# Optimization experiments

Hardware: AMD Instinct MI355X
Metric: run time of the kernel (lower is better)

Reference implementation:

```python
import jax, jax.numpy as jnp
import numpy as np

N = 100000
IN_DIM = 128
HID = 32
HEADS = 2
DEG = 16
NEG_SLOPE = 0.2


def setup_inputs() -> dict:
    rng = np.random.default_rng(0)
    E_rand = N * DEG
    src = np.concatenate([rng.integers(0, N, E_rand), np.arange(N)]).astype(np.int64)
    dst = np.concatenate([rng.integers(0, N, E_rand), np.arange(N)]).astype(np.int64)

    key = jax.random.key(0)
    ks = jax.random.split(key, 10)
    feat = jax.random.normal(ks[0], (N, IN_DIM), dtype=jnp.float32)
    # layer 1: in_dim -> HEADS * HID
    W1 = jax.random.normal(ks[1], (IN_DIM, HEADS * HID), dtype=jnp.float32) / np.sqrt(IN_DIM)
    al1 = jax.random.normal(ks[2], (HEADS, HID), dtype=jnp.float32) * 0.1
    ar1 = jax.random.normal(ks[3], (HEADS, HID), dtype=jnp.float32) * 0.1
    b1 = jnp.zeros((HEADS * HID,), dtype=jnp.float32)
    # layer 2: HEADS*HID -> 1 * HID
    W2 = jax.random.normal(ks[4], (HEADS * HID, HID), dtype=jnp.float32) / np.sqrt(HEADS * HID)
    al2 = jax.random.normal(ks[5], (1, HID), dtype=jnp.float32) * 0.1
    ar2 = jax.random.normal(ks[6], (1, HID), dtype=jnp.float32) * 0.1
    b2 = jnp.zeros((HID,), dtype=jnp.float32)
    return {"feat": feat, "W1": W1, "al1": al1, "ar1": ar1, "b1": b1,
            "W2": W2, "al2": al2, "ar2": ar2, "b2": b2,
            "src": jnp.asarray(src), "dst": jnp.asarray(dst)}


def gat_conv(feat, W, al, ar, b, src, dst, n_nodes, activation=True):
    # DGL GATConv: fc (no bias) -> per-head dot with attn vecs -> leaky_relu
    # edge score -> softmax over incoming edges of each dst -> scatter-add -> +bias -> relu
    H, D = al.shape
    h = (feat @ W).reshape(-1, H, D)                       # [N,H,D]
    el = jnp.einsum('nhd,hd->nh', h, al)                   # [N,H]
    er = jnp.einsum('nhd,hd->nh', h, ar)                   # [N,H]
    e = jax.nn.leaky_relu(el[src] + er[dst], NEG_SLOPE)    # [E,H]
    m = jax.ops.segment_max(e, dst, num_segments=n_nodes)  # [N,H]
    e = jnp.exp(e - jax.lax.stop_gradient(m)[dst])
    s = jax.ops.segment_sum(e, dst, num_segments=n_nodes)  # [N,H]
    a = e / s[dst]                                         # [E,H]
    msg = h[src] * a[:, :, None]                           # [E,H,D]
    out = jax.ops.segment_sum(msg, dst, num_segments=n_nodes)  # [N,H,D]
    out = out + b.reshape(1, H, D)
    return jax.nn.relu(out) if activation else out


def reference(feat, W1, al1, ar1, b1, W2, al2, ar2, b2, src, dst):
    h = gat_conv(feat, W1, al1, ar1, b1, src, dst, N)      # [N,HEADS,HID]
    h = h.reshape(h.shape[0], -1)                          # [N,HEADS*HID]
    h = gat_conv(h, W2, al2, ar2, b2, src, dst, N)         # [N,1,HID]
    return h.squeeze(1)                                    # [N,HID]
```

## Files before the change

### kernel.cpp

```cpp
#include <hip/hip_runtime.h>
#include <hip/hip_fp16.h>
#include <math.h>


constexpr int CAP  = 64;
constexpr int MAXB = 512;
constexpr int TILE = 2048;
constexpr int BCAP = 5120;

typedef _Float16 f16x8 __attribute__((ext_vector_type(8)));
typedef float    f32x4 __attribute__((ext_vector_type(4)));

__global__ __launch_bounds__(256)
void k_prew(const float* __restrict__ W1, const float* __restrict__ al1, const float* __restrict__ ar1,
            const float* __restrict__ W2, const float* __restrict__ al2, const float* __restrict__ ar2,
            _Float16* __restrict__ vh1, _Float16* __restrict__ B2h, int* __restrict__ gcur)
{
    const int t = threadIdx.x;
    for (int i = t; i < 128 * 16; i += 256) {
        const int k = i >> 4, c = i & 15;
        float s = 0.f;
        if (c < 4) {
            const int h = c & 1;
            const float* a = (c >> 1) ? ar1 : al1;
            #pragma unroll
            for (int d = 0; d < 32; d++) s += W1[k * 64 + h * 32 + d] * a[h * 32 + d];
        }
        vh1[i] = (_Float16)s;
    }
    for (int i = t; i < 64 * 64; i += 256) {
        const int k = i >> 6, c = i & 63;
        float s = 0.f;
        if (c < 32) s = W2[k * 32 + c];
        else if (c < 34) {
            const float* a = (c == 32) ? al2 : ar2;
            #pragma unroll
            for (int d = 0; d < 32; d++) s += W2[k * 32 + d] * a[d];
        }
        B2h[i] = (_Float16)s;
    }
    for (int b = t; b < MAXB; b += 256) gcur[b] = 0;
}

__global__ __launch_bounds__(256)
void k_front(const int* __restrict__ src, const int* __restrict__ dst,
             int* __restrict__ gcur, unsigned* __restrict__ binbuf, int E, int Gbin,
             const float* __restrict__ x, const float* __restrict__ W,
             const _Float16* __restrict__ vh1,
             __half* __restrict__ h1, float* __restrict__ el, float* __restrict__ er,
             int nnodes)
{
    __shared__ alignas(16) char smem[32 * 1024];
    const int tid = threadIdx.x;

    if ((int)blockIdx.x < Gbin) {
        int* cnt  = (int*)smem;
        int* base = cnt + MAXB;
        for (int b = tid; b < MAXB; b += 256) cnt[b] = 0;
        __syncthreads();
        const int e0 = blockIdx.x * TILE;
        int lo[8]; unsigned rec[8]; int bn[8];
        #pragma unroll
        for (int u = 0; u < 8; u++) {
            const int e = e0 + u * 256 + tid;
            if (e < E) {
                const int d = dst[e];
                bn[u]  = d >> 8;
                rec[u] = ((unsigned)src[e] << 8) | (unsigned)(d & 255);
                lo[u]  = atomicAdd(&cnt[bn[u]], 1);
            } else bn[u] = -1;
        }
        __syncthreads();
        for (int b = tid; b < MAXB; b += 256) {
            const int c = cnt[b];
            base[b] = c ? atomicAdd(&gcur[b], c) : 0;
        }
        __syncthreads();
        #pragma unroll
        for (int u = 0; u < 8; u++) if (bn[u] >= 0) {
            const int p = base[bn[u]] + lo[u];
            if ((unsigned)p < (unsigned)BCAP)
                binbuf[(long)bn[u] * BCAP + p] = rec[u];
        }
        return;
    }

    _Float16* xs = (_Float16*)smem;
    _Float16* Wh = xs + 64 * 128;
    const int node0 = ((int)blockIdx.x - Gbin) * 64;

    for (int c = tid; c < 1024; c += 256) {
        const int row = c >> 4, k8 = c & 15;
        const int n = node0 + row;
        float4 v0 = make_float4(0, 0, 0, 0), v1 = v0;
        if (n < nnodes) {
            v0 = ((const float4*)x)[(long)n * 32 + k8 * 2];
            v1 = ((const float4*)x)[(long)n * 32 + k8 * 2 + 1];
        }
        f16x8 h;
        h[0] = v0.x; h[1] = v0.y; h[2] = v0.z; h[3] = v0.w;
        h[4] = v1.x; h[5] = v1.y; h[6] = v1.z; h[7] = v1.w;
        const int off = (row * 256 + k8 * 16) ^ ((row & 7) << 4);
        *(f16x8*)((char*)xs + off) = h;
    }
    for (int c = tid; c < 1024; c += 256) {
        const int k = c >> 3, j8 = (c & 7) * 8;
        float4 v0 = ((const float4*)W)[(k * 64 + j8) >> 2];
        float4 v1 = ((const float4*)W)[((k * 64 + j8) >> 2) + 1];
        f16x8 h;
        h[0] = v0.x; h[1] = v0.y; h[2] = v0.z; h[3] = v0.w;
        h[4] = v1.x; h[5] = v1.y; h[6] = v1.z; h[7] = v1.w;
        *(f16x8*)(Wh + k * 64 + j8) = h;
    }
    __syncthreads();

    const int wv = tid >> 6, l = tid & 63;
    const int col = wv * 16 + (l & 15);
    const int g = l >> 4;
    f16x8 bfr[4], vfr[4];
    #pragma unroll
    for (int t = 0; t < 4; t++)
        #pragma unroll
        for (int e = 0; e < 8; e++)
            bfr[t][e] = Wh[(t * 32 + g * 8 + e) * 64 + col];
    if (wv == 0) {
        #pragma unroll
        for (int t = 0; t < 4; t++)
            #pragma unroll
            for (int e = 0; e < 8; e++)
                vfr[t][e] = vh1[(t * 32 + g * 8 + e) * 16 + (l & 15)];
    }

    #pragma unroll
    for (int nt = 0; nt < 4; nt++) {
        f32x4 acc = {0.f, 0.f, 0.f, 0.f}, accv = {0.f, 0.f, 0.f, 0.f};
        const int row = nt * 16 + (l & 15);
        #pragma unroll
        for (int t = 0; t < 4; t++) {
            const int off = (row * 256 + (t * 32 + g * 8) * 2) ^ ((row & 7) << 4);
            f16x8 af = *(const f16x8*)((const char*)xs + off);
            acc = __builtin_amdgcn_mfma_f32_16x16x32_f16(af, bfr[t], acc, 0, 0, 0);
            if (wv == 0)
                accv = __builtin_amdgcn_mfma_f32_16x16x32_f16(af, vfr[t], accv, 0, 0, 0);
        }
        #pragma unroll
        for (int r = 0; r < 4; r++) {
            const int n = node0 + nt * 16 + g * 4 + r;
            if (n < nnodes) {
                h1[(long)n * 64 + col] = __float2half((float)acc[r]);
                if (wv == 0) {
                    const int c4 = l & 15;
                    if (c4 < 2)      el[n * 2 + c4]       = (float)accv[r];
                    else if (c4 < 4) er[n * 2 + (c4 - 2)] = (float)accv[r];
                }
            }
        }
    }
}

__global__ __launch_bounds__(256)
void k_scatter(const unsigned* __restrict__ binbuf, const int* __restrict__ gcur,
               int* __restrict__ deg, int* __restrict__ bucket, int nnodes)
{
    extern __shared__ int lds[];
    int* ldeg  = lds;
    int* lbuck = lds + 256;
    const int t = threadIdx.x, b = blockIdx.x;
    const int nb0 = b << 8;
    ldeg[t] = 0;
    __syncthreads();
    const int cnt = min(max(gcur[b], 0), BCAP);
    const unsigned* recs = binbuf + (long)b * BCAP;
    for (int i = t; i < cnt; i += 256) {
        const unsigned r = recs[i];
        const int nl  = (int)(r & 255u);
        const int pos = atomicAdd(&ldeg[nl], 1);
        if (pos < CAP) lbuck[nl * CAP + pos] = (int)(r >> 8);
    }
    __syncthreads();
    const int nv = min(256, nnodes - nb0);
    if (t < nv) deg[nb0 + t] = ldeg[t];
    const int tot4 = nv * (CAP / 4);
    int4* gb = (int4*)(bucket + (long)nb0 * CAP);
    const int4* lb = (const int4*)lbuck;
    for (int i = t; i < tot4; i += 256) gb[i] = lb[i];
}

__global__ __launch_bounds__(256)
void k_agg1(const __half* __restrict__ hbuf, const float* __restrict__ el,
            const float* __restrict__ er, const int* __restrict__ deg,
            const int* __restrict__ bucket, const float* __restrict__ b1,
            __half* __restrict__ o1, int nnodes)
{
    constexpr int OUT = 64;
    const int w = threadIdx.x >> 6, lane = threadIdx.x & 63;
    const int n = blockIdx.x * 4 + w;
    __shared__ int    sbuf[4][CAP];
    __shared__ float2 wbuf[4][CAP];
    if (n >= nnodes) return;

    const int dn = min(deg[n], CAP);
    const int sv = (lane < dn) ? bucket[(long)n * CAP + lane] : 0;
    sbuf[w][lane] = sv;

    const float2 ernv = ((const float2*)er)[n];
    const float2 elv  = ((const float2*)el)[sv];
    float e0 = elv.x + ernv.x; e0 = (e0 > 0.f) ? e0 : 0.2f * e0;
    float e1 = elv.y + ernv.y; e1 = (e1 > 0.f) ? e1 : 0.2f * e1;
    const float w0 = (lane < dn) ? __expf(e0) : 0.f;
    const float w1 = (lane < dn) ? __expf(e1) : 0.f;
    wbuf[w][lane] = make_float2(w0, w1);
    float s0 = w0, s1 = w1;
    #pragma unroll
    for (int off = 32; off; off >>= 1) {
        s0 += __shfl_xor(s0, off, 64);
        s1 += __shfl_xor(s1, off, 64);
    }
    const float inv0 = (s0 > 0.f) ? 1.f / s0 : 0.f;
    const float inv1 = (s1 > 0.f) ? 1.f / s1 : 0.f;

    const int q = lane >> 3, c8 = lane & 7, hh = c8 >> 2;
    const float invC = hh ? inv1 : inv0;
    float acc[8] = {0.f,0.f,0.f,0.f,0.f,0.f,0.f,0.f};
    for (int i = 0; i < dn; i += 16) {
        const int   sA = sbuf[w][i + q],                     sB = sbuf[w][i + 8 + q];
        const float wA = ((const float*)&wbuf[w][i + q])[hh];
        const float wB = ((const float*)&wbuf[w][i + 8 + q])[hh];
        union { float4 f4; __half2 h2v[4]; } uA, uB;
        uA.f4 = *(const float4*)(hbuf + (long)sA * OUT + c8 * 8);
        uB.f4 = *(const float4*)(hbuf + (long)sB * OUT + c8 * 8);
        #pragma unroll
        for (int j = 0; j < 4; j++) {
            const float2 xa = __half22float2(uA.h2v[j]);
            const float2 xb = __half22float2(uB.h2v[j]);
            acc[2*j]   = fmaf(xa.x, wA, acc[2*j]);
            acc[2*j+1] = fmaf(xa.y, wA, acc[2*j+1]);
            acc[2*j]   = fmaf(xb.x, wB, acc[2*j]);
            acc[2*j+1] = fmaf(xb.y, wB, acc[2*j+1]);
        }
    }
    #pragma unroll
    for (int j = 0; j < 8; j++) {
        acc[j] += __shfl_xor(acc[j], 8, 64);
        acc[j] += __shfl_xor(acc[j], 16, 64);
        acc[j] += __shfl_xor(acc[j], 32, 64);
    }
    if (q == 0) {
        f16x8 ov;
        #pragma unroll
        for (int j = 0; j < 8; j++)
            ov[j] = (_Float16)fmaxf(acc[j] * invC + b1[c8 * 8 + j], 0.f);
        *(f16x8*)((char*)o1 + (long)n * 128 + c8 * 16) = ov;
    }
}

__global__ __launch_bounds__(256)
void k_gemm2(const __half* __restrict__ o1, const _Float16* __restrict__ B2h,
             __half* __restrict__ h2, float* __restrict__ el2, float* __restrict__ er2,
             int nnodes)
{
    __shared__ _Float16 xs[64 * 64];
    const int tid = threadIdx.x;
    const int node0 = blockIdx.x * 64;

    for (int c = tid; c < 512; c += 256) {
        const int row = c >> 3, k8 = c & 7;
        const int n = node0 + row;
        f16x8 h = {0,0,0,0,0,0,0,0};
        if (n < nnodes) h = *(const f16x8*)((const char*)o1 + (long)n * 128 + k8 * 16);
        const int off = (row * 128 + k8 * 16) ^ ((row & 7) << 4);
        *(f16x8*)((char*)xs + off) = h;
    }
    __syncthreads();

    const int wv = tid >> 6, l = tid & 63;
    if (wv == 3) return;
    const int col = wv * 16 + (l & 15);
    const int g = l >> 4;
    f16x8 bfr[2];
    #pragma unroll
    for (int t = 0; t < 2; t++)
        #pragma unroll
        for (int e = 0; e < 8; e++)
            bfr[t][e] = B2h[(t * 32 + g * 8 + e) * 64 + col];

    #pragma unroll
    for (int nt = 0; nt < 4; nt++) {
        f32x4 acc = {0.f, 0.f, 0.f, 0.f};
        const int row = nt * 16 + (l & 15);
        #pragma unroll
        for (int t = 0; t < 2; t++) {
            const int off = (row * 128 + (t * 32 + g * 8) * 2) ^ ((row & 7) << 4);
            f16x8 af = *(const f16x8*)((const char*)xs + off);
            acc = __builtin_amdgcn_mfma_f32_16x16x32_f16(af, bfr[t], acc, 0, 0, 0);
        }
        #pragma unroll
        for (int r = 0; r < 4; r++) {
            const int n = node0 + nt * 16 + g * 4 + r;
            if (n < nnodes) {
                if (wv < 2) h2[(long)n * 32 + col] = __float2half((float)acc[r]);
                else {
                    const int c4 = l & 15;
                    if (c4 == 0)      el2[n] = (float)acc[r];
                    else if (c4 == 1) er2[n] = (float)acc[r];
                }
            }
        }
    }
}

__global__ __launch_bounds__(256)
void k_agg2(const __half* __restrict__ h2, const float* __restrict__ el2,
            const float* __restrict__ er2, const int* __restrict__ deg,
            const int* __restrict__ bucket, const float* __restrict__ b2,
            float* __restrict__ out, int nnodes)
{
    const int w = threadIdx.x >> 6, lane = threadIdx.x & 63;
    const int n = blockIdx.x * 4 + w;
    __shared__ int   sbuf[4][CAP];
    __shared__ float wbuf[4][CAP];
    if (n >= nnodes) return;

    const int dn = min(deg[n], CAP);
    const int sv = (lane < dn) ? bucket[(long)n * CAP + lane] : 0;
    sbuf[w][lane] = sv;

    const float ern = er2[n];
    float e = el2[sv] + ern; e = (e > 0.f) ? e : 0.2f * e;
    const float wt = (lane < dn) ? __expf(e) : 0.f;
    wbuf[w][lane] = wt;
    float s = wt;
    #pragma unroll
    for (int off = 32; off; off >>= 1) s += __shfl_xor(s, off, 64);
    const float inv = (s > 0.f) ? 1.f / s : 0.f;

    const int q = lane >> 2, c8 = lane & 3;
    float acc[8] = {0.f,0.f,0.f,0.f,0.f,0.f,0.f,0.f};
    for (int i = 0; i < dn; i += 16) {
        const int   sA = sbuf[w][i + q];
        const float wA = wbuf[w][i + q];
        union { float4 f4; __half2 h2v[4]; } uA;
        uA.f4 = *(const float4*)(h2 + (long)sA * 32 + c8 * 8);
        #pragma unroll
        for (int j = 0; j < 4; j++) {
            const float2 xa = __half22float2(uA.h2v[j]);
            acc[2*j]   = fmaf(xa.x, wA, acc[2*j]);
            acc[2*j+1] = fmaf(xa.y, wA, acc[2*j+1]);
        }
    }
    #pragma unroll
    for (int j = 0; j < 8; j++) {
        acc[j] += __shfl_xor(acc[j], 4, 64);
        acc[j] += __shfl_xor(acc[j], 8, 64);
        acc[j] += __shfl_xor(acc[j], 16, 64);
        acc[j] += __shfl_xor(acc[j], 32, 64);
    }
    if (q == 0) {
        float r[8];
        #pragma unroll
        for (int j = 0; j < 8; j++)
            r[j] = fmaxf(acc[j] * inv + b2[c8 * 8 + j], 0.f);
        float4* po = (float4*)(out + (long)n * 32 + c8 * 8);
        po[0] = make_float4(r[0], r[1], r[2], r[3]);
        po[1] = make_float4(r[4], r[5], r[6], r[7]);
    }
}

extern "C" void kernel_launch(void* const* d_in, const int* in_sizes, int n_in,
                              void* d_out, int out_size, void* d_ws, size_t ws_size,
                              hipStream_t stream)
{
    const float* feat = (const float*)d_in[0];
    const float* W1   = (const float*)d_in[1];
    const float* al1  = (const float*)d_in[2];
    const float* ar1  = (const float*)d_in[3];
    const float* b1   = (const float*)d_in[4];
    const float* W2   = (const float*)d_in[5];
    const float* al2  = (const float*)d_in[6];
    const float* ar2  = (const float*)d_in[7];
    const float* b2   = (const float*)d_in[8];
    const int*   src  = (const int*)d_in[9];
    const int*   dst  = (const int*)d_in[10];

    const int N  = in_sizes[0] / 128;
    const int E  = in_sizes[9];
    const int NB = (N + 255) >> 8;

    char* ws = (char*)d_ws;
    size_t off = 0;
    auto alloc = [&](size_t bytes) -> void* {
        void* p = ws + off;
        off += (bytes + 255) & ~size_t(255);
        return p;
    };
    const size_t szA = ((size_t)NB * BCAP * 4 > (size_t)N * 64 * 2)
                     ? (size_t)NB * BCAP * 4 : (size_t)N * 64 * 2;
    char*     A      = (char*)    alloc(szA);
    unsigned* binbuf = (unsigned*)A;
    __half*   o1     = (__half*)  A;
    char*     B      = (char*)    alloc((size_t)N * 64 * 2);
    __half*   h1     = (__half*)  B;
    __half*   h2     = (__half*)  B;
    int*      gcur   = (int*)     alloc((size_t)MAXB * 4);
    int*      deg    = (int*)     alloc((size_t)N * 4);
    int*      bucket = (int*)     alloc((size_t)N * CAP * 4);
    float*    el1    = (float*)   alloc((size_t)N * 2 * 4);
    float*    er1    = (float*)   alloc((size_t)N * 2 * 4);
    float*    el2    = (float*)   alloc((size_t)N * 4);
    float*    er2    = (float*)   alloc((size_t)N * 4);
    _Float16* vh1    = (_Float16*)alloc(128 * 16 * 2);
    _Float16* B2h    = (_Float16*)alloc(64 * 64 * 2);

    const int Gbin  = (E + TILE - 1) / TILE;
    const int Ggemm = (N + 63) / 64;

    k_prew<<<1, 256, 0, stream>>>(W1, al1, ar1, W2, al2, ar2, vh1, B2h, gcur);
    k_front<<<Gbin + Ggemm, 256, 0, stream>>>(src, dst, gcur, binbuf, E, Gbin,
                                              feat, W1, vh1, h1, el1, er1, N);
    k_scatter<<<NB, 256, (256 + 256 * CAP) * 4, stream>>>(binbuf, gcur, deg, bucket, N);
    k_agg1<<<(N + 3) / 4, 256, 0, stream>>>(h1, el1, er1, deg, bucket, b1, o1, N);
    k_gemm2<<<(N + 63) / 64, 256, 0, stream>>>(o1, B2h, h2, el2, er2, N);
    k_agg2<<<(N + 3) / 4, 256, 0, stream>>>(h2, el2, er2, deg, bucket, b2,
                                            (float*)d_out, N);
}
```

Before: 281.7 us.

## Replace padded per-node bucket array with compact CSR adjacency

The scatter kernel now does a block-wide prefix scan of per-node degrees and reserves a contiguous range with a global atomic. It then writes neighbor lists compactly into an E-sized adjacency array, with an (offset, degree) descriptor per node. The goal is to cut the write and read traffic of the padded N*64 bucket array. The cost is a serial scan in scatter and per-thread strided edge writes, and node ranges now land in nondeterministic block order.

```diff
diff --git a/kernel.cpp b/kernel.cpp
--- a/kernel.cpp
+++ b/kernel.cpp
@@ -39,7 +39,7 @@
         }
         B2h[i] = (_Float16)s;
     }
-    for (int b = t; b < MAXB; b += 256) gcur[b] = 0;
+    for (int b = t; b < MAXB + 1; b += 256) gcur[b] = 0;
 }
 
 __global__ __launch_bounds__(256)
@@ -159,12 +159,14 @@
 }
 
 __global__ __launch_bounds__(256)
-void k_scatter(const unsigned* __restrict__ binbuf, const int* __restrict__ gcur,
-               int* __restrict__ deg, int* __restrict__ bucket, int nnodes)
+void k_scatter(const unsigned* __restrict__ binbuf, int* __restrict__ gcur,
+               int2* __restrict__ ndesc, int* __restrict__ eadj, int nnodes)
 {
     extern __shared__ int lds[];
     int* ldeg  = lds;
-    int* lbuck = lds + 256;
+    int* lscan = lds + 256;
+    int* lbuck = lds + 512;
+    __shared__ int sbase;
     const int t = threadIdx.x, b = blockIdx.x;
     const int nb0 = b << 8;
     ldeg[t] = 0;
@@ -175,21 +177,31 @@
         const unsigned r = recs[i];
         const int nl  = (int)(r & 255u);
         const int pos = atomicAdd(&ldeg[nl], 1);
-        if (pos < CAP) lbuck[nl * CAP + pos] = (int)(r >> 8);
-    }
-    __syncthreads();
-    const int nv = min(256, nnodes - nb0);
-    if (t < nv) deg[nb0 + t] = ldeg[t];
-    const int tot4 = nv * (CAP / 4);
-    int4* gb = (int4*)(bucket + (long)nb0 * CAP);
-    const int4* lb = (const int4*)lbuck;
-    for (int i = t; i < tot4; i += 256) gb[i] = lb[i];
+        if (pos < CAP) lbuck[pos * 256 + nl] = (int)(r >> 8);
+    }
+    __syncthreads();
+    const int dn = min(ldeg[t], CAP);
+    lscan[t] = dn;
+    __syncthreads();
+    for (int o = 1; o < 256; o <<= 1) {
+        const int v = lscan[t];
+        const int u = (t >= o) ? lscan[t - o] : 0;
+        __syncthreads();
+        lscan[t] = v + u;
+        __syncthreads();
+    }
+    if (t == 0) sbase = atomicAdd(&gcur[MAXB], lscan[255]);
+    __syncthreads();
+    const int start = sbase + lscan[t] - dn;
+    const int n = nb0 + t;
+    if (n < nnodes) ndesc[n] = make_int2(start, dn);
+    for (int i = 0; i < dn; i++) eadj[start + i] = lbuck[i * 256 + t];
 }
 
 __global__ __launch_bounds__(256)
 void k_agg1(const __half* __restrict__ hbuf, const float* __restrict__ el,
-            const float* __restrict__ er, const int* __restrict__ deg,
-            const int* __restrict__ bucket, const float* __restrict__ b1,
+            const float* __restrict__ er, const int2* __restrict__ ndesc,
+            const int* __restrict__ eadj, const float* __restrict__ b1,
             __half* __restrict__ o1, int nnodes)
 {
     constexpr int OUT = 64;
@@ -199,8 +211,9 @@
     __shared__ float2 wbuf[4][CAP];
     if (n >= nnodes) return;
 
-    const int dn = min(deg[n], CAP);
-    const int sv = (lane < dn) ? bucket[(long)n * CAP + lane] : 0;
+    const int2 nd = ndesc[n];
+    const int dn = nd.y;
+    const int sv = (lane < dn) ? eadj[nd.x + lane] : 0;
     sbuf[w][lane] = sv;
 
     const float2 ernv = ((const float2*)er)[n];
@@ -311,8 +324,8 @@
 
 __global__ __launch_bounds__(256)
 void k_agg2(const __half* __restrict__ h2, const float* __restrict__ el2,
-            const float* __restrict__ er2, const int* __restrict__ deg,
-            const int* __restrict__ bucket, const float* __restrict__ b2,
+            const float* __restrict__ er2, const int2* __restrict__ ndesc,
+            const int* __restrict__ eadj, const float* __restrict__ b2,
             float* __restrict__ out, int nnodes)
 {
     const int w = threadIdx.x >> 6, lane = threadIdx.x & 63;
@@ -321,8 +334,9 @@
     __shared__ float wbuf[4][CAP];
     if (n >= nnodes) return;
 
-    const int dn = min(deg[n], CAP);
-    const int sv = (lane < dn) ? bucket[(long)n * CAP + lane] : 0;
+    const int2 nd = ndesc[n];
+    const int dn = nd.y;
+    const int sv = (lane < dn) ? eadj[nd.x + lane] : 0;
     sbuf[w][lane] = sv;
 
     const float ern = er2[n];
@@ -398,12 +412,12 @@
     char*     A      = (char*)    alloc(szA);
     unsigned* binbuf = (unsigned*)A;
     __half*   o1     = (__half*)  A;
-    char*     B      = (char*)    alloc((size_t)N * 64 * 2);
-    __half*   h1     = (__half*)  B;
-    __half*   h2     = (__half*)  B;
-    int*      gcur   = (int*)     alloc((size_t)MAXB * 4);
-    int*      deg    = (int*)     alloc((size_t)N * 4);
-    int*      bucket = (int*)     alloc((size_t)N * CAP * 4);
+    char*     Br     = (char*)    alloc((size_t)N * 64 * 2);
+    __half*   h1     = (__half*)  Br;
+    __half*   h2     = (__half*)  Br;
+    int*      gcur   = (int*)     alloc((size_t)(MAXB + 1) * 4);
+    int2*     ndesc  = (int2*)    alloc((size_t)N * 8);
+    int*      eadj   = (int*)     alloc((size_t)E * 4);
     float*    el1    = (float*)   alloc((size_t)N * 2 * 4);
     float*    er1    = (float*)   alloc((size_t)N * 2 * 4);
     float*    el2    = (float*)   alloc((size_t)N * 4);
@@ -417,9 +431,9 @@
     k_prew<<<1, 256, 0, stream>>>(W1, al1, ar1, W2, al2, ar2, vh1, B2h, gcur);
     k_front<<<Gbin + Ggemm, 256, 0, stream>>>(src, dst, gcur, binbuf, E, Gbin,
                                               feat, W1, vh1, h1, el1, er1, N);
-    k_scatter<<<NB, 256, (256 + 256 * CAP) * 4, stream>>>(binbuf, gcur, deg, bucket, N);
-    k_agg1<<<(N + 3) / 4, 256, 0, stream>>>(h1, el1, er1, deg, bucket, b1, o1, N);
+    k_scatter<<<NB, 256, (512 + 256 * CAP) * 4, stream>>>(binbuf, gcur, ndesc, eadj, N);
+    k_agg1<<<(N + 3) / 4, 256, 0, stream>>>(h1, el1, er1, ndesc, eadj, b1, o1, N);
     k_gemm2<<<(N + 63) / 64, 256, 0, stream>>>(o1, B2h, h2, el2, er2, N);
-    k_agg2<<<(N + 3) / 4, 256, 0, stream>>>(h2, el2, er2, deg, bucket, b2,
+    k_agg2<<<(N + 3) / 4, 256, 0, stream>>>(h2, el2, er2, ndesc, eadj, b2,
                                             (float*)d_out, N);
 }
```

Measured after the change: 293.7 us. +4.3%, slower.
